# Kernel tuning notes

Measured on AMD Instinct MI355X. Metric: run time of the kernel, lower is better.

Reference implementation:

```python
import jax, jax.numpy as jnp
import numpy as np

N, D, H = 500000, 128, 128
B, M = 1024, 512


def setup_inputs() -> dict:
    key = jax.random.key(0)
    k = jax.random.split(key, 8)
    return {
        "embed": jax.random.normal(k[0], (N, D), dtype=jnp.float32),
        "node_feat": jax.random.normal(k[1], (N, D), dtype=jnp.float32),
        "W1": jax.random.normal(k[2], (2 * D, H), dtype=jnp.float32) * 0.05,
        "b1": jnp.zeros((H,), dtype=jnp.float32),
        "W2": jax.random.normal(k[3], (H, 1), dtype=jnp.float32) * 0.05,
        "b2": jnp.zeros((1,), dtype=jnp.float32),
        "query_idx": jax.random.randint(k[4], (B,), 0, N),
        "cand_idx": jax.random.randint(k[5], (B, M), 0, N),
        "top_k": 3,
    }


def reference(embed, node_feat, W1, b1, W2, b2, query_idx, cand_idx, top_k):
    # Gather query and candidate (k-hop subgraph) embeddings.
    q = embed[query_idx]                                   # [B, D]
    c = embed[cand_idx]                                    # [B, M, D]
    Bv, Mv, Dv = c.shape
    pair = jnp.concatenate(
        [jnp.broadcast_to(q[:, None, :], (Bv, Mv, Dv)), c], axis=-1
    )                                                      # [B, M, 2D]
    # Tiny 2-layer MLP edge scorer (one fused pass over all edges).
    h = jax.nn.relu(jnp.einsum("bmf,fh->bmh", pair, W1) + b1)
    scores = (jnp.einsum("bmh,ho->bmo", h, W2) + b2)[..., 0]  # [B, M]
    # Sort-based top-k selection (original sorted per-etype lists).
    _, pos = jax.lax.top_k(scores, top_k)                  # [B, k]
    top_nodes = jnp.take_along_axis(cand_idx, pos, axis=1) # [B, k]
    # Zero out features of the selected nodes (hard mask), as in original.
    masked_feat = node_feat.at[top_nodes.reshape(-1)].set(0.0)
    return scores, masked_feat
```

## Files before the change

kernel.cpp:

```cpp
#include <hip/hip_runtime.h>
#include <math.h>

#define D 128
#define H 128
#define BQ 1024
#define M 512
#define NNODES 500000
#define K_MAX 8
#define SHORT 16
#define NSCORE (BQ * 2)
#define NCOPY 2048
#define COPY_N4 ((long)NNODES * D / 4)

typedef __attribute__((ext_vector_type(8))) short bf16x8;
typedef __attribute__((ext_vector_type(4))) float f32x4;
typedef __attribute__((ext_vector_type(4))) unsigned u32x4;

static __device__ __forceinline__ unsigned pack2bf(float a, float b) {
    unsigned ua = __float_as_uint(a);
    unsigned ub = __float_as_uint(b);
    ua = ua + 0x7fffu + ((ua >> 16) & 1u);
    ub = ub + 0x7fffu + ((ub >> 16) & 1u);
    return (ua >> 16) | (ub & 0xffff0000u);
}

__global__ void wconv_kernel(const float* __restrict__ W1,
                             unsigned short* __restrict__ wTswz) {
    const int idx = blockIdx.x * 256 + threadIdx.x;
    const int h = idx >> 7;
    const int inner = (idx & 127) * 2;
    const int k = (inner ^ ((h & 15) << 4)) >> 1;
    const float v = W1[(long)(D + k) * H + h];
    wTswz[idx] = (unsigned short)pack2bf(v, 0.f);
}

__global__ void qproj_kernel(const float* __restrict__ embed,
                             const float* __restrict__ W1,
                             const float* __restrict__ b1,
                             const int* __restrict__ query_idx,
                             float* __restrict__ qh) {
    __shared__ float qrow[D];
    const int b = blockIdx.x;
    const int t = threadIdx.x;
    const long qi = query_idx[b];
    qrow[t] = embed[qi * D + t];
    __syncthreads();
    float acc = b1[t];
#pragma unroll 8
    for (int d = 0; d < D; ++d)
        acc = fmaf(qrow[d], W1[d * H + t], acc);
    qh[b * H + t] = acc;
}

__global__ __launch_bounds__(256, 5)
void score_kernel(const float* __restrict__ embed,
                  const unsigned short* __restrict__ wTswz,
                  const float* __restrict__ W2,
                  const float* __restrict__ b2,
                  const int* __restrict__ cand_idx,
                  const float* __restrict__ qh,
                  float* __restrict__ scores) {
    __shared__ __align__(16) char Bs[32768];
    const int bid = blockIdx.x;
    const int t   = threadIdx.x;
    const int b    = bid >> 1;
    const int half = bid & 1;

    {
#pragma unroll
        for (int i = 0; i < 8; ++i) {
            const int c = i * 256 + t;
            const uint4 v = ((const uint4*)wTswz)[c];
            *(uint4*)(Bs + (size_t)c * 16) = v;
        }
    }

    const int lane = t & 63;
    const int w    = t >> 6;
    const int g    = lane >> 4;
    const int c    = lane & 15;
    const int sw   = c << 4;

    float qv[8], w2[8];
#pragma unroll
    for (int cb = 0; cb < 8; ++cb) {
        qv[cb] = qh[b * H + cb * 16 + c];
        w2[cb] = W2[cb * 16 + c];
    }
    const float b2v = b2[0];

    int idx[4];
    const int ibase = b * M + half * 256 + w * 16 + c;
#pragma unroll
    for (int mt = 0; mt < 4; ++mt) idx[mt] = cand_idx[ibase + mt * 64];

    __syncthreads();

    f32x4 buf[8];
    {
        const float* rp = embed + (long)idx[0] * D + g * 8;
#pragma unroll
        for (int ks = 0; ks < 4; ++ks) {
            buf[2 * ks]     = *(const f32x4*)(rp + ks * 32);
            buf[2 * ks + 1] = *(const f32x4*)(rp + ks * 32 + 4);
        }
    }

#pragma unroll
    for (int mt = 0; mt < 4; ++mt) {
        bf16x8 afr[4];
#pragma unroll
        for (int ks = 0; ks < 4; ++ks) {
            u32x4 u;
            u.x = pack2bf(buf[2 * ks].x, buf[2 * ks].y);
            u.y = pack2bf(buf[2 * ks].z, buf[2 * ks].w);
            u.z = pack2bf(buf[2 * ks + 1].x, buf[2 * ks + 1].y);
            u.w = pack2bf(buf[2 * ks + 1].z, buf[2 * ks + 1].w);
            afr[ks] = __builtin_bit_cast(bf16x8, u);
        }
        if (mt < 3) {
            const float* rp = embed + (long)idx[mt + 1] * D + g * 8;
#pragma unroll
            for (int ks = 0; ks < 4; ++ks) {
                buf[2 * ks]     = *(const f32x4*)(rp + ks * 32);
                buf[2 * ks + 1] = *(const f32x4*)(rp + ks * 32 + 4);
            }
        }

        f32x4 acc[8];
#pragma unroll
        for (int cb = 0; cb < 8; ++cb) acc[cb] = (f32x4){0.f, 0.f, 0.f, 0.f};
#pragma unroll
        for (int ks = 0; ks < 4; ++ks) {
            const int koff = (ks * 64 + g * 16) ^ sw;
#pragma unroll
            for (int cb = 0; cb < 8; ++cb) {
                const bf16x8 bv = *(const bf16x8*)(Bs + ((cb * 16 + c) << 8) + koff);
                acc[cb] = __builtin_amdgcn_mfma_f32_16x16x32_bf16(afr[ks], bv, acc[cb], 0, 0, 0);
            }
        }

        float s0 = 0.f, s1 = 0.f, s2 = 0.f, s3 = 0.f;
#pragma unroll
        for (int cb = 0; cb < 8; ++cb) {
            s0 = fmaf(fmaxf(qv[cb] + acc[cb][0], 0.f), w2[cb], s0);
            s1 = fmaf(fmaxf(qv[cb] + acc[cb][1], 0.f), w2[cb], s1);
            s2 = fmaf(fmaxf(qv[cb] + acc[cb][2], 0.f), w2[cb], s2);
            s3 = fmaf(fmaxf(qv[cb] + acc[cb][3], 0.f), w2[cb], s3);
        }
#pragma unroll
        for (int off = 1; off <= 8; off <<= 1) {
            s0 += __shfl_xor(s0, off);
            s1 += __shfl_xor(s1, off);
            s2 += __shfl_xor(s2, off);
            s3 += __shfl_xor(s3, off);
        }
        if (c == 0) {
            float* out = scores + b * M + half * 256 + mt * 64 + w * 16 + g * 4;
            out[0] = s0 + b2v;
            out[1] = s1 + b2v;
            out[2] = s2 + b2v;
            out[3] = s3 + b2v;
        }
    }
}

__global__ void topk16_kernel(const float* __restrict__ scores,
                              int* __restrict__ shortpos) {
    const int b = blockIdx.x;
    const int lane = threadIdx.x;
    const float* row = scores + b * M;
    float v[8];
    {
        const float4 x0 = ((const float4*)row)[lane * 2];
        const float4 x1 = ((const float4*)row)[lane * 2 + 1];
        v[0] = x0.x; v[1] = x0.y; v[2] = x0.z; v[3] = x0.w;
        v[4] = x1.x; v[5] = x1.y; v[6] = x1.z; v[7] = x1.w;
    }
    for (int kk = 0; kk < SHORT; ++kk) {
        float bv = v[0];
        int bi = lane * 8;
#pragma unroll
        for (int j = 1; j < 8; ++j)
            if (v[j] > bv) { bv = v[j]; bi = lane * 8 + j; }
#pragma unroll
        for (int off = 32; off >= 1; off >>= 1) {
            const float ov = __shfl_xor(bv, off);
            const int   oi = __shfl_xor(bi, off);
            if (ov > bv || (ov == bv && oi < bi)) { bv = ov; bi = oi; }
        }
        if (lane == 0) shortpos[b * SHORT + kk] = bi;
        if ((bi >> 3) == lane) v[bi & 7] = -3.402823466e38f;
    }
}

__global__ __launch_bounds__(128)
void refine_kernel(const float* __restrict__ embed,
                   const float* __restrict__ W1,
                   const float* __restrict__ W2,
                   const float* __restrict__ qh,
                   const int* __restrict__ cand_idx,
                   const int* __restrict__ shortpos,
                   const int* __restrict__ topk_ptr,
                   int* __restrict__ top_nodes) {
    __shared__ float crows[SHORT][D];
    __shared__ float red[SHORT][D];
    __shared__ int spos[SHORT];
    const int b = blockIdx.x;
    const int t = threadIdx.x;

    if (t < SHORT) spos[t] = shortpos[b * SHORT + t];
    __syncthreads();
    {
        const int cc = t >> 3;
        const int d0 = (t & 7) * 16;
        const long node = cand_idx[b * M + spos[cc]];
        const float4* rp = (const float4*)(embed + node * D);
        float4* wp = (float4*)&crows[cc][d0];
#pragma unroll
        for (int j = 0; j < 4; ++j) wp[j] = rp[d0 / 4 + j];
    }
    __syncthreads();

    float acc[SHORT];
#pragma unroll
    for (int cc = 0; cc < SHORT; ++cc) acc[cc] = 0.f;
    const float* W1bot = W1 + (long)D * H;
    for (int d = 0; d < D; ++d) {
        const float w1v = W1bot[d * H + t];
#pragma unroll
        for (int cc = 0; cc < SHORT; ++cc)
            acc[cc] = fmaf(crows[cc][d], w1v, acc[cc]);
    }
    const float qv = qh[b * H + t];
    const float w2 = W2[t];
#pragma unroll
    for (int cc = 0; cc < SHORT; ++cc)
        red[cc][t] = fmaxf(qv + acc[cc], 0.f) * w2;
    __syncthreads();

    if (t < 64) {
#pragma unroll
        for (int cc = 0; cc < SHORT; ++cc) {
            float v = red[cc][t] + red[cc][t + 64];
#pragma unroll
            for (int off = 32; off >= 1; off >>= 1) v += __shfl_xor(v, off);
            if (t == 0) red[cc][0] = v;
        }
    }
    __syncthreads();

    if (t == 0) {
        int k = *topk_ptr;
        if (k > K_MAX) k = K_MAX;
        unsigned used = 0;
        for (int kk = 0; kk < K_MAX; ++kk) {
            if (kk < k) {
                int best = -1, bpos = 0x7fffffff;
                float bv = 0.f;
                for (int cc = 0; cc < SHORT; ++cc) {
                    if (used & (1u << cc)) continue;
                    const float v = red[cc][0];
                    const int p = spos[cc];
                    if (best < 0 || v > bv || (v == bv && p < bpos)) {
                        best = cc; bv = v; bpos = p;
                    }
                }
                used |= 1u << best;
                top_nodes[b * K_MAX + kk] = cand_idx[b * M + bpos];
            } else {
                top_nodes[b * K_MAX + kk] = -1;
            }
        }
    }
}

__global__ void copy_kernel(const f32x4* __restrict__ src,
                            f32x4* __restrict__ dst, long n4) {
    long i = (long)blockIdx.x * blockDim.x + threadIdx.x;
    const long stride = (long)gridDim.x * blockDim.x;
    for (; i < n4; i += stride) {
        const f32x4 v = __builtin_nontemporal_load(&src[i]);
        __builtin_nontemporal_store(v, &dst[i]);
    }
}

__global__ void zero_rows_kernel(const int* __restrict__ top_nodes,
                                 float* __restrict__ masked) {
    const int node = top_nodes[blockIdx.x];
    if (node < 0) return;
    masked[(long)node * D + threadIdx.x] = 0.f;
}

extern "C" void kernel_launch(void* const* d_in, const int* in_sizes, int n_in,
                              void* d_out, int out_size, void* d_ws, size_t ws_size,
                              hipStream_t stream) {
    const float* embed     = (const float*)d_in[0];
    const float* node_feat = (const float*)d_in[1];
    const float* W1        = (const float*)d_in[2];
    const float* b1        = (const float*)d_in[3];
    const float* W2        = (const float*)d_in[4];
    const float* b2        = (const float*)d_in[5];
    const int*   query_idx = (const int*)d_in[6];
    const int*   cand_idx  = (const int*)d_in[7];
    const int*   topk_ptr  = (const int*)d_in[8];

    float* scores = (float*)d_out;
    float* masked = (float*)d_out + (long)BQ * M;

    char* p = (char*)d_ws;
    float*          qh        = (float*)p;          p += (long)BQ * H * 4;
    int*            shortpos  = (int*)p;            p += (long)BQ * SHORT * 4;
    int*            top_nodes = (int*)p;            p += (long)BQ * K_MAX * 4;
    unsigned short* wTswz     = (unsigned short*)p;

    wconv_kernel<<<(H * D) / 256, 256, 0, stream>>>(W1, wTswz);
    qproj_kernel<<<BQ, H, 0, stream>>>(embed, W1, b1, query_idx, qh);

    score_kernel<<<NSCORE, 256, 0, stream>>>(embed, wTswz, W2, b2,
                                             cand_idx, qh, scores);

    topk16_kernel<<<BQ, 64, 0, stream>>>(scores, shortpos);
    refine_kernel<<<BQ, 128, 0, stream>>>(embed, W1, W2, qh, cand_idx,
                                          shortpos, topk_ptr, top_nodes);

    copy_kernel<<<NCOPY, 256, 0, stream>>>((const f32x4*)node_feat,
                                           (f32x4*)masked, COPY_N4);
    zero_rows_kernel<<<BQ * K_MAX, D, 0, stream>>>(top_nodes, masked);
}
```

Measured before the change: 211.3 us.

## Fuse node-feature copy into score kernel and read weights from global

```diff
diff --git a/kernel.cpp b/kernel.cpp
--- a/kernel.cpp
+++ b/kernel.cpp
@@ -25,13 +25,12 @@
 }
 
 __global__ void wconv_kernel(const float* __restrict__ W1,
-                             unsigned short* __restrict__ wTswz) {
+                             unsigned short* __restrict__ wT) {
     const int idx = blockIdx.x * 256 + threadIdx.x;
     const int h = idx >> 7;
-    const int inner = (idx & 127) * 2;
-    const int k = (inner ^ ((h & 15) << 4)) >> 1;
+    const int k = idx & 127;
     const float v = W1[(long)(D + k) * H + h];
-    wTswz[idx] = (unsigned short)pack2bf(v, 0.f);
+    wT[idx] = (unsigned short)pack2bf(v, 0.f);
 }
 
 __global__ void qproj_kernel(const float* __restrict__ embed,
@@ -52,34 +51,38 @@
     qh[b * H + t] = acc;
 }
 
-__global__ __launch_bounds__(256, 5)
-void score_kernel(const float* __restrict__ embed,
-                  const unsigned short* __restrict__ wTswz,
+__global__ __launch_bounds__(256, 8)
+void fused_kernel(const float* __restrict__ embed,
+                  const unsigned short* __restrict__ wT,
                   const float* __restrict__ W2,
                   const float* __restrict__ b2,
                   const int* __restrict__ cand_idx,
                   const float* __restrict__ qh,
-                  float* __restrict__ scores) {
-    __shared__ __align__(16) char Bs[32768];
+                  float* __restrict__ scores,
+                  const f32x4* __restrict__ nf_src,
+                  f32x4* __restrict__ nf_dst) {
     const int bid = blockIdx.x;
     const int t   = threadIdx.x;
-    const int b    = bid >> 1;
-    const int half = bid & 1;
-
-    {
-#pragma unroll
-        for (int i = 0; i < 8; ++i) {
-            const int c = i * 256 + t;
-            const uint4 v = ((const uint4*)wTswz)[c];
-            *(uint4*)(Bs + (size_t)c * 16) = v;
-        }
-    }
+
+    if ((bid & 1) == 0) {
+        const int cid = bid >> 1;
+        long i = (long)cid * 256 + t;
+        const long stride = (long)NCOPY * 256;
+        for (; i < COPY_N4; i += stride) {
+            const f32x4 v = __builtin_nontemporal_load(&nf_src[i]);
+            __builtin_nontemporal_store(v, &nf_dst[i]);
+        }
+        return;
+    }
+
+    const int sid  = bid >> 1;
+    const int b    = sid >> 1;
+    const int half = sid & 1;
 
     const int lane = t & 63;
     const int w    = t >> 6;
     const int g    = lane >> 4;
     const int c    = lane & 15;
-    const int sw   = c << 4;
 
     float qv[8], w2[8];
 #pragma unroll
@@ -94,7 +97,7 @@
 #pragma unroll
     for (int mt = 0; mt < 4; ++mt) idx[mt] = cand_idx[ibase + mt * 64];
 
-    __syncthreads();
+    const char* wbase = (const char*)wT;
 
     f32x4 buf[8];
     {
@@ -131,11 +134,11 @@
 #pragma unroll
         for (int cb = 0; cb < 8; ++cb) acc[cb] = (f32x4){0.f, 0.f, 0.f, 0.f};
 #pragma unroll
-        for (int ks = 0; ks < 4; ++ks) {
-            const int koff = (ks * 64 + g * 16) ^ sw;
-#pragma unroll
-            for (int cb = 0; cb < 8; ++cb) {
-                const bf16x8 bv = *(const bf16x8*)(Bs + ((cb * 16 + c) << 8) + koff);
+        for (int cb = 0; cb < 8; ++cb) {
+            const char* bp = wbase + ((cb * 16 + c) << 8) + (g << 4);
+#pragma unroll
+            for (int ks = 0; ks < 4; ++ks) {
+                const bf16x8 bv = *(const bf16x8*)(bp + ks * 64);
                 acc[cb] = __builtin_amdgcn_mfma_f32_16x16x32_bf16(afr[ks], bv, acc[cb], 0, 0, 0);
             }
         }
@@ -275,16 +278,6 @@
     }
 }
 
-__global__ void copy_kernel(const f32x4* __restrict__ src,
-                            f32x4* __restrict__ dst, long n4) {
-    long i = (long)blockIdx.x * blockDim.x + threadIdx.x;
-    const long stride = (long)gridDim.x * blockDim.x;
-    for (; i < n4; i += stride) {
-        const f32x4 v = __builtin_nontemporal_load(&src[i]);
-        __builtin_nontemporal_store(v, &dst[i]);
-    }
-}
-
 __global__ void zero_rows_kernel(const int* __restrict__ top_nodes,
                                  float* __restrict__ masked) {
     const int node = top_nodes[blockIdx.x];
@@ -312,19 +305,17 @@
     float*          qh        = (float*)p;          p += (long)BQ * H * 4;
     int*            shortpos  = (int*)p;            p += (long)BQ * SHORT * 4;
     int*            top_nodes = (int*)p;            p += (long)BQ * K_MAX * 4;
-    unsigned short* wTswz     = (unsigned short*)p;
-
-    wconv_kernel<<<(H * D) / 256, 256, 0, stream>>>(W1, wTswz);
+    unsigned short* wT        = (unsigned short*)p;
+
+    wconv_kernel<<<(H * D) / 256, 256, 0, stream>>>(W1, wT);
     qproj_kernel<<<BQ, H, 0, stream>>>(embed, W1, b1, query_idx, qh);
 
-    score_kernel<<<NSCORE, 256, 0, stream>>>(embed, wTswz, W2, b2,
-                                             cand_idx, qh, scores);
+    fused_kernel<<<NSCORE + NCOPY, 256, 0, stream>>>(
+        embed, wT, W2, b2, cand_idx, qh, scores,
+        (const f32x4*)node_feat, (f32x4*)masked);
 
     topk16_kernel<<<BQ, 64, 0, stream>>>(scores, shortpos);
     refine_kernel<<<BQ, 128, 0, stream>>>(embed, W1, W2, qh, cand_idx,
                                           shortpos, topk_ptr, top_nodes);
-
-    copy_kernel<<<NCOPY, 256, 0, stream>>>((const f32x4*)node_feat,
-                                           (f32x4*)masked, COPY_N4);
     zero_rows_kernel<<<BQ * K_MAX, D, 0, stream>>>(top_nodes, masked);
 }
```

After: 555.5 us. 2.63x slower.
